# Kernel tuning notes

Hardware: AMD Instinct MI355X
Metric: run time of the kernel (lower is better)

## Reference

```python
import math
import jax, jax.numpy as jnp
import numpy as np

C_S, C_Z, N_HEAD, C, N_QP, N_PV = 384, 128, 12, 16, 4, 8
B, N_RES = 1, 512
OUT_IN = N_HEAD * (C + 3 * N_PV + N_PV + C_Z)  # 2112


def _quat_to_rot(q):
    # q: (..., 4) unit quaternions -> (..., 3, 3) rotation matrices
    w, x, y, z = q[..., 0], q[..., 1], q[..., 2], q[..., 3]
    R = jnp.stack([
        1 - 2 * (y * y + z * z), 2 * (x * y - w * z), 2 * (x * z + w * y),
        2 * (x * y + w * z), 1 - 2 * (x * x + z * z), 2 * (y * z - w * x),
        2 * (x * z - w * y), 2 * (y * z + w * x), 1 - 2 * (x * x + y * y),
    ], axis=-1)
    return R.reshape(q.shape[:-1] + (3, 3))


def setup_inputs() -> dict:
    key = jax.random.key(0)
    ks = jax.random.split(key, 16)
    s = jax.random.normal(ks[0], (B, N_RES, C_S), jnp.float32)
    z = jax.random.normal(ks[1], (B, N_RES, N_RES, C_Z), jnp.float32)
    # Valid rigid backbone transforms: random rotation + translation in 4x4 homogeneous form.
    quat = jax.random.normal(ks[2], (B, N_RES, 4), jnp.float32)
    quat = quat / jnp.linalg.norm(quat, axis=-1, keepdims=True)
    R = _quat_to_rot(quat)
    t = 10.0 * jax.random.normal(ks[3], (B, N_RES, 3), jnp.float32)
    T = jnp.zeros((B, N_RES, 4, 4), jnp.float32)
    T = T.at[..., :3, :3].set(R).at[..., :3, 3].set(t).at[..., 3, 3].set(1.0)
    sc = 0.02
    w_q = sc * jax.random.normal(ks[4], (C_S, N_HEAD * C), jnp.float32)
    w_k = sc * jax.random.normal(ks[5], (C_S, N_HEAD * C), jnp.float32)
    w_v = sc * jax.random.normal(ks[6], (C_S, N_HEAD * C), jnp.float32)
    w_qp = sc * jax.random.normal(ks[7], (C_S, N_HEAD * N_QP * 3), jnp.float32)
    w_kp = sc * jax.random.normal(ks[8], (C_S, N_HEAD * N_QP * 3), jnp.float32)
    w_vp = sc * jax.random.normal(ks[9], (C_S, N_HEAD * N_PV * 3), jnp.float32)
    w_b = sc * jax.random.normal(ks[10], (C_Z, N_HEAD), jnp.float32)
    gamma = 0.5 * jax.random.normal(ks[11], (N_HEAD,), jnp.float32)
    w_out = sc * jax.random.normal(ks[12], (OUT_IN, C_S), jnp.float32)
    b_out = jnp.zeros((C_S,), jnp.float32)
    return dict(s=s, z=z, T=T, w_q=w_q, w_k=w_k, w_v=w_v, w_qp=w_qp, w_kp=w_kp,
                w_vp=w_vp, w_b=w_b, gamma=gamma, w_out=w_out, b_out=b_out)


def _ipa(s, z, T, w_q, w_k, w_v, w_qp, w_kp, w_vp, w_b, gamma, w_out, b_out):
    b, n, _ = s.shape
    H, c, P, Pv = N_HEAD, C, N_QP, N_PV
    # qkv embeddings: (b, H, n, c)
    q = (s @ w_q).reshape(b, n, H, c).transpose(0, 2, 1, 3)
    k = (s @ w_k).reshape(b, n, H, c).transpose(0, 2, 1, 3)
    v = (s @ w_v).reshape(b, n, H, c).transpose(0, 2, 1, 3)
    # point embeddings: (b, H, P, n, 3)
    qp = (s @ w_qp).reshape(b, n, H, P, 3).transpose(0, 2, 3, 1, 4)
    kp = (s @ w_kp).reshape(b, n, H, P, 3).transpose(0, 2, 3, 1, 4)
    vp = (s @ w_vp).reshape(b, n, H, Pv, 3).transpose(0, 2, 3, 1, 4)
    R = T[..., :3, :3]                      # (b, n, 3, 3)
    t = T[..., :3, 3]                       # (b, n, 3)
    t_b = t[:, None, None, :, :]            # broadcast over (H, P)
    # global-frame points: T_i o x = R_i x + t_i
    qpg = jnp.einsum('bnxy,bhpny->bhpnx', R, qp) + t_b
    kpg = jnp.einsum('bnxy,bhpny->bhpnx', R, kp) + t_b
    vpg = jnp.einsum('bnxy,bhpny->bhpnx', R, vp) + t_b
    # attention logits (Alg 22 line 7)
    bias = jnp.einsum('bijz,zh->bhij', z, w_b)                      # pair bias
    dot = jnp.einsum('bhic,bhjc->bhij', q, k) * (1.0 / math.sqrt(c))
    diff = qpg[:, :, :, :, None, :] - kpg[:, :, :, None, :, :]       # (b,H,P,i,j,3)
    d2 = jnp.sum(diff * diff, axis=(2, 5))                           # (b,H,i,j)
    gamma_sp = jax.nn.softplus(gamma)[None, :, None, None]
    w_C = math.sqrt(2.0 / (9.0 * P))
    w_L = math.sqrt(1.0 / 3.0)
    a = jax.nn.softmax(w_L * (dot + bias - 0.5 * gamma_sp * w_C * d2), axis=-1)
    # outputs
    o = jnp.einsum('bhij,bhjc->bhic', a, v)                          # (b,H,n,c)
    opg = jnp.einsum('bhij,bhpjx->bhpix', a, vpg)                    # (b,H,Pv,n,3)
    # back to local frame: T_i^{-1} o x = R_i^T (x - t_i)
    op = jnp.einsum('bnxy,bhpnx->bhpny', R, opg - t_b)
    op_norm = jnp.sqrt(jnp.sum(op * op, axis=-1) + 1e-8)             # (b,H,Pv,n)
    o_pair = jnp.einsum('bhij,bijz->bhiz', a, z)                     # (b,H,n,c_z)
    o_f = o.transpose(0, 2, 1, 3).reshape(b, n, H * c)
    op_f = op.transpose(0, 3, 1, 2, 4).reshape(b, n, H * Pv * 3)
    norm_f = op_norm.transpose(0, 3, 1, 2).reshape(b, n, H * Pv)
    pair_f = o_pair.transpose(0, 2, 1, 3).reshape(b, n, H * C_Z)
    cat = jnp.concatenate([o_f, op_f, norm_f, pair_f], axis=-1)      # (b, n, OUT_IN)
    return cat @ w_out + b_out


def reference(s, z, T, w_q, w_k, w_v, w_qp, w_kp, w_vp, w_b, gamma, w_out, b_out):
    return _ipa(s, z, T, w_q, w_k, w_v, w_qp, w_kp, w_vp, w_b, gamma, w_out, b_out)
```

## Files before the change

kernel.cpp:

```cpp
#include <hip/hip_runtime.h>
#include <hip/hip_bf16.h>

typedef __attribute__((ext_vector_type(8))) short short8v;
typedef __attribute__((ext_vector_type(4))) float f32x4;

__device__ __forceinline__ short f2bf(float f){
  unsigned u = __builtin_bit_cast(unsigned, f);
  u += 0x7fffu + ((u >> 16) & 1u);
  return (short)(u >> 16);
}
__device__ __forceinline__ float bf2f(unsigned short s){
  unsigned u = ((unsigned)s) << 16;
  return __builtin_bit_cast(float, u);
}

__device__ __forceinline__ void gload16(const short* g, short* l){
  __builtin_amdgcn_global_load_lds(
    (const __attribute__((address_space(1))) unsigned int*)g,
    (__attribute__((address_space(3))) unsigned int*)l,
    16, 0, 0);
}

__global__ __launch_bounds__(256) void prep_kernel(
    const float* __restrict__ s, const float* __restrict__ w_b,
    const float* __restrict__ wq, const float* __restrict__ wk, const float* __restrict__ wv,
    const float* __restrict__ wqp, const float* __restrict__ wkp, const float* __restrict__ wvp,
    const float* __restrict__ w_out,
    short* __restrict__ s_bf, short* __restrict__ wbbf,
    short* __restrict__ WT, short* __restrict__ w_outT)
{
  __shared__ float tsh[64][65];
  int b = blockIdx.x;
  if (b < 192) {
    int gid = b*256 + threadIdx.x;
    float4 f = *(const float4*)(s + (size_t)gid*4);
    short4 o = make_short4(f2bf(f.x), f2bf(f.y), f2bf(f.z), f2bf(f.w));
    *(short4*)(s_bf + (size_t)gid*4) = o;
  } else if (b == 192) {
    const float wL = 0.57735026918962576f;
    for (int u = threadIdx.x; u < 2048; u += 256) {
      int h = u >> 7, zc = u & 127;
      float v = (h < 12) ? w_b[zc*12 + h]*wL : 0.f;
      wbbf[u] = f2bf(v);
    }
  } else if (b < 373) {
    int t = b - 193;
    int n0 = (t % 5)*64, k0 = ((t/5) % 6)*64, src = t/30;
    const float* in; int N; int rowoff;
    switch (src) {
      case 0: in = wq;  N = 192; rowoff = 0;   break;
      case 1: in = wk;  N = 192; rowoff = 192; break;
      case 2: in = wv;  N = 192; rowoff = 384; break;
      case 3: in = wqp; N = 144; rowoff = 576; break;
      case 4: in = wkp; N = 144; rowoff = 720; break;
      default:in = wvp; N = 288; rowoff = 864; break;
    }
    if (n0 >= N) return;
    int lx = threadIdx.x & 15, ly = threadIdx.x >> 4;
    #pragma unroll
    for (int p=0;p<4;++p){
      int r = ly + p*16, c = lx*4;
      float v0=0.f,v1=0.f,v2=0.f,v3=0.f;
      if (n0 + c + 3 < N) {
        float4 v = *(const float4*)(in + (size_t)(k0+r)*N + n0 + c);
        v0=v.x; v1=v.y; v2=v.z; v3=v.w;
      } else {
        if (n0+c+0 < N) v0 = in[(size_t)(k0+r)*N + n0+c+0];
        if (n0+c+1 < N) v1 = in[(size_t)(k0+r)*N + n0+c+1];
        if (n0+c+2 < N) v2 = in[(size_t)(k0+r)*N + n0+c+2];
        if (n0+c+3 < N) v3 = in[(size_t)(k0+r)*N + n0+c+3];
      }
      tsh[c+0][r]=v0; tsh[c+1][r]=v1; tsh[c+2][r]=v2; tsh[c+3][r]=v3;
    }
    __syncthreads();
    #pragma unroll
    for (int p=0;p<4;++p){
      int nr = ly + p*16, kc = lx*4;
      if (n0 + nr < N) {
        short4 o = make_short4(f2bf(tsh[nr][kc]), f2bf(tsh[nr][kc+1]),
                               f2bf(tsh[nr][kc+2]), f2bf(tsh[nr][kc+3]));
        *(short4*)(WT + (size_t)(rowoff+n0+nr)*384 + k0 + kc) = o;
      }
    }
  } else {
    int t = b - 373;
    int n0 = (t % 6)*64, k0 = (t/6)*64;
    int lx = threadIdx.x & 15, ly = threadIdx.x >> 4;
    #pragma unroll
    for (int p=0;p<4;++p){
      int r = ly + p*16, c = lx*4;
      float4 v = *(const float4*)(w_out + (size_t)(k0+r)*384 + n0 + c);
      tsh[c+0][r]=v.x; tsh[c+1][r]=v.y; tsh[c+2][r]=v.z; tsh[c+3][r]=v.w;
    }
    __syncthreads();
    #pragma unroll
    for (int p=0;p<4;++p){
      int nr = ly + p*16, kc = lx*4;
      short4 o = make_short4(f2bf(tsh[nr][kc]), f2bf(tsh[nr][kc+1]),
                             f2bf(tsh[nr][kc+2]), f2bf(tsh[nr][kc+3]));
      *(short4*)(w_outT + (size_t)(n0+nr)*2112 + k0 + kc) = o;
    }
  }
}

__global__ __launch_bounds__(256) void gemm_bf16_kernel(
    const short* __restrict__ A, const short* __restrict__ BT,
    float* __restrict__ C, const float* __restrict__ bias,
    int M, int N, int K)
{
  __shared__ __align__(16) short As[2][4096];
  __shared__ __align__(16) short Bs[2][4096];
  int tid = threadIdx.x;
  int n0 = blockIdx.x*128, m0 = blockIdx.y*128;
  int w = tid >> 6, lane = tid & 63;
  int wr = w >> 1, wc = w & 1;
  int lrow = lane & 15, kg = lane >> 4;
  int nt = K >> 5;
  f32x4 acc[4][4] = {};

  const short* Abase = A  + (size_t)m0*K;
  const short* Bbase = BT + (size_t)n0*K;
  int sr = tid >> 2, scc = (tid & 3)*8;

  auto stage = [&](int b, int k0){
    const short* Ab = Abase + k0;
    const short* Bb = Bbase + k0;
    gload16(Ab + (size_t)sr*K + scc,      &As[b][tid*8]);
    gload16(Bb + (size_t)sr*K + scc,      &Bs[b][tid*8]);
    gload16(Ab + (size_t)(sr+64)*K + scc, &As[b][2048 + tid*8]);
    gload16(Bb + (size_t)(sr+64)*K + scc, &Bs[b][2048 + tid*8]);
  };

  stage(0, 0);
  for (int kt = 0; kt < nt; ++kt){
    int cb = kt & 1;
    if (kt + 1 < nt){
      stage(cb ^ 1, (kt+1) << 5);
      asm volatile("s_waitcnt vmcnt(4)" ::: "memory");
    } else {
      asm volatile("s_waitcnt vmcnt(0)" ::: "memory");
    }
    __builtin_amdgcn_s_barrier();
    short8v af[4], bfr[4];
    #pragma unroll
    for (int mi=0; mi<4; ++mi)
      af[mi]  = *(const short8v*)&As[cb][(wr*64 + mi*16 + lrow)*32 + kg*8];
    #pragma unroll
    for (int ni=0; ni<4; ++ni)
      bfr[ni] = *(const short8v*)&Bs[cb][(wc*64 + ni*16 + lrow)*32 + kg*8];
    #pragma unroll
    for (int mi=0; mi<4; ++mi)
      #pragma unroll
      for (int ni=0; ni<4; ++ni)
        acc[mi][ni] = __builtin_amdgcn_mfma_f32_16x16x32_bf16(af[mi], bfr[ni], acc[mi][ni], 0, 0, 0);
    __builtin_amdgcn_s_barrier();
  }

  #pragma unroll
  for (int mi=0; mi<4; ++mi)
    #pragma unroll
    for (int ni=0; ni<4; ++ni) {
      int col = n0 + wc*64 + ni*16 + lrow;
      float bv = bias ? bias[col] : 0.f;
      #pragma unroll
      for (int jj=0; jj<4; ++jj) {
        int row = m0 + wr*64 + mi*16 + kg*4 + jj;
        C[(size_t)row*N + col] = acc[mi][ni][jj] + bv;
      }
    }
}

__global__ __launch_bounds__(256) void gemm_splitk_kernel(
    const short* __restrict__ A, const short* __restrict__ BT,
    float* __restrict__ Cpart, int M, int N, int lda, int Kc)
{
  __shared__ __align__(16) short As[2][4096];
  __shared__ __align__(16) short Bs[2][4096];
  int tid = threadIdx.x;
  int n0 = blockIdx.x*128, m0 = blockIdx.y*128;
  int kb = blockIdx.z;
  int w = tid >> 6, lane = tid & 63;
  int wr = w >> 1, wc = w & 1;
  int lrow = lane & 15, kg = lane >> 4;
  int nt = Kc >> 5;
  f32x4 acc[4][4] = {};

  const short* Abase = A  + (size_t)m0*lda + (size_t)kb*Kc;
  const short* Bbase = BT + (size_t)n0*lda + (size_t)kb*Kc;
  int sr = tid >> 2, scc = (tid & 3)*8;

  auto stage = [&](int b, int k0){
    const short* Ab = Abase + k0;
    const short* Bb = Bbase + k0;
    gload16(Ab + (size_t)sr*lda + scc,      &As[b][tid*8]);
    gload16(Bb + (size_t)sr*lda + scc,      &Bs[b][tid*8]);
    gload16(Ab + (size_t)(sr+64)*lda + scc, &As[b][2048 + tid*8]);
    gload16(Bb + (size_t)(sr+64)*lda + scc, &Bs[b][2048 + tid*8]);
  };

  stage(0, 0);
  for (int kt = 0; kt < nt; ++kt){
    int cb = kt & 1;
    if (kt + 1 < nt){
      stage(cb ^ 1, (kt+1) << 5);
      asm volatile("s_waitcnt vmcnt(4)" ::: "memory");
    } else {
      asm volatile("s_waitcnt vmcnt(0)" ::: "memory");
    }
    __builtin_amdgcn_s_barrier();
    short8v af[4], bfr[4];
    #pragma unroll
    for (int mi=0; mi<4; ++mi)
      af[mi]  = *(const short8v*)&As[cb][(wr*64 + mi*16 + lrow)*32 + kg*8];
    #pragma unroll
    for (int ni=0; ni<4; ++ni)
      bfr[ni] = *(const short8v*)&Bs[cb][(wc*64 + ni*16 + lrow)*32 + kg*8];
    #pragma unroll
    for (int mi=0; mi<4; ++mi)
      #pragma unroll
      for (int ni=0; ni<4; ++ni)
        acc[mi][ni] = __builtin_amdgcn_mfma_f32_16x16x32_bf16(af[mi], bfr[ni], acc[mi][ni], 0, 0, 0);
    __builtin_amdgcn_s_barrier();
  }

  float* Cp = Cpart + (size_t)kb*M*N;
  #pragma unroll
  for (int mi=0; mi<4; ++mi)
    #pragma unroll
    for (int ni=0; ni<4; ++ni) {
      int col = n0 + wc*64 + ni*16 + lrow;
      #pragma unroll
      for (int jj=0; jj<4; ++jj) {
        int row = m0 + wr*64 + mi*16 + kg*4 + jj;
        Cp[(size_t)row*N + col] = acc[mi][ni][jj];
      }
    }
}

__global__ __launch_bounds__(256) void reduce6_kernel(
    const float* __restrict__ Cpart, const float* __restrict__ bias,
    float* __restrict__ out)
{
  int idx = blockIdx.x*256 + threadIdx.x;
  float v = bias[idx % 384];
  #pragma unroll
  for (int zc = 0; zc < 6; ++zc) v += Cpart[(size_t)zc*196608 + idx];
  out[idx] = v;
}

__global__ __launch_bounds__(256) void transform_kernel(
    const float* __restrict__ P, const float* __restrict__ T,
    float* __restrict__ kT, float* __restrict__ kpgT,
    float* __restrict__ qpg, unsigned short* __restrict__ vcatT)
{
  __shared__ float Ps[8][1160];
  __shared__ float Ts[8][12];
  int tid = threadIdx.x;
  int j0 = blockIdx.x*8;
  for (int u = tid; u < 8*288; u += 256) {
    int r = u / 288, c4 = u % 288;
    *(float4*)&Ps[r][c4*4] = *(const float4*)(P + (size_t)(j0+r)*1152 + c4*4);
  }
  if (tid < 96) {
    int r = tid / 12, e = tid % 12;
    Ts[r][e] = (e < 9) ? T[(j0+r)*16 + (e/3)*4 + (e%3)]
                       : T[(j0+r)*16 + (e-9)*4 + 3];
  }
  __syncthreads();
  for (int u = tid; u < 1536; u += 256) {
    int row = u >> 3, jl = u & 7;
    kT[(size_t)row*512 + j0 + jl] = Ps[jl][192 + row];
  }
  for (int u = tid; u < 1152; u += 256) {
    int e = u >> 3, jl = u & 7;
    int x = e % 3, hp = e / 3;
    const float* R = &Ts[jl][0];
    float kx = Ps[jl][720+hp*3], ky = Ps[jl][720+hp*3+1], kz = Ps[jl][720+hp*3+2];
    kpgT[(size_t)e*512 + j0 + jl] = R[x*3]*kx + R[x*3+1]*ky + R[x*3+2]*kz + Ts[jl][9+x];
  }
  for (int u = tid; u < 1152; u += 256) {
    int jl = u / 144, e = u % 144;
    int x = e % 3, hp = e / 3;
    const float* R = &Ts[jl][0];
    float qx = Ps[jl][576+hp*3], qy = Ps[jl][576+hp*3+1], qz = Ps[jl][576+hp*3+2];
    qpg[(size_t)(j0+jl)*144 + e] = R[x*3]*qx + R[x*3+1]*qy + R[x*3+2]*qz + Ts[jl][9+x];
  }
  for (int u = tid; u < 3840; u += 256) {
    int d = u >> 3, jl = u & 7;
    float val;
    if (d < 192) val = Ps[jl][384 + d];
    else {
      int e = d - 192;
      int x = e % 3, hp = e / 3;
      const float* R = &Ts[jl][0];
      float vx = Ps[jl][864+hp*3], vy = Ps[jl][864+hp*3+1], vz = Ps[jl][864+hp*3+2];
      val = R[x*3]*vx + R[x*3+1]*vy + R[x*3+2]*vz + Ts[jl][9+x];
    }
    vcatT[(size_t)d*512 + j0 + jl] = (unsigned short)f2bf(val);
  }
}

__global__ __launch_bounds__(256) void attn_part_kernel(
    const float* __restrict__ P, const float* __restrict__ qpg,
    const float* __restrict__ kT, const float* __restrict__ kpgT,
    const short* __restrict__ wbbf, const float* __restrict__ z,
    const unsigned short* __restrict__ vcatT,
    const float* __restrict__ gamma, float* __restrict__ part)
{
  __shared__ short zbT[16384];
  __shared__ float sc[12][132];
  __shared__ float qrow[192], qpgrow[144], gsp[12];
  int bid = blockIdx.x;
  int i = bid >> 2, jq = bid & 3;
  int j0 = jq * 128;
  int tid = threadIdx.x;
  float* pb = part + (size_t)bid * 2048;
  const float* zslab = z + (size_t)i*65536 + (size_t)j0*128;

  if (tid < 192) qrow[tid] = P[(size_t)i*1152 + tid];
  if (tid < 144) qpgrow[tid] = qpg[(size_t)i*144 + tid];
  if (tid < 12)  { float g = gamma[tid]; gsp[tid] = log1pf(__expf(g)); }

  {
    int q = tid & 31, jb = tid >> 5;
    for (int r = 0; r < 16; ++r) {
      int jj = jb + r*8;
      float4 f = *(const float4*)(zslab + (size_t)jj*128 + q*4);
      short wv0 = f2bf(f.x), wv1 = f2bf(f.y), wv2 = f2bf(f.z), wv3 = f2bf(f.w);
      int jc = jj >> 3, jr = jj & 7;
      int zc = q*4;
      zbT[(zc+0)*128 + ((jc ^ (((zc+0)&15)^((zc+0)>>4))) << 3) + jr] = wv0;
      zbT[(zc+1)*128 + ((jc ^ (((zc+1)&15)^((zc+1)>>4))) << 3) + jr] = wv1;
      zbT[(zc+2)*128 + ((jc ^ (((zc+2)&15)^((zc+2)>>4))) << 3) + jr] = wv2;
      zbT[(zc+3)*128 + ((jc ^ (((zc+3)&15)^((zc+3)>>4))) << 3) + jr] = wv3;
    }
  }

  {
    int w = tid >> 6, lane = tid & 63;
    int lrow = lane & 15, kg = lane >> 4;
    #pragma unroll
    for (int sub = 0; sub < 2; ++sub) {
      int m = w*2 + sub;
      const float* zr = zslab + (size_t)(m*16 + lrow)*128;
      f32x4 acc = {0.f,0.f,0.f,0.f};
      #pragma unroll
      for (int ks = 0; ks < 4; ++ks) {
        int c0 = ks*32 + kg*8;
        float4 z0 = *(const float4*)(zr + c0);
        float4 z1 = *(const float4*)(zr + c0 + 4);
        short8v af;
        af[0]=f2bf(z0.x); af[1]=f2bf(z0.y); af[2]=f2bf(z0.z); af[3]=f2bf(z0.w);
        af[4]=f2bf(z1.x); af[5]=f2bf(z1.y); af[6]=f2bf(z1.z); af[7]=f2bf(z1.w);
        short8v bfv = *(const short8v*)(wbbf + lrow*128 + c0);
        acc = __builtin_amdgcn_mfma_f32_16x16x32_bf16(af, bfv, acc, 0, 0, 0);
      }
      if (lrow < 12) {
        #pragma unroll
        for (int r=0;r<4;++r)
          sc[lrow][m*16 + kg*4 + r] = acc[r];
      }
    }
  }
  __syncthreads();

  {
    int j = tid & 127, hh = tid >> 7;
    const float wL = 0.57735026918962576f;
    const float wC = 0.23570226039551584f;
    #pragma unroll
    for (int hl = 0; hl < 6; ++hl) {
      int h = hh*6 + hl;
      float dot = 0.f;
      #pragma unroll
      for (int c=0;c<16;++c) dot += qrow[h*16+c] * kT[(size_t)(h*16+c)*512 + j0 + j];
      float d2 = 0.f;
      #pragma unroll
      for (int e=0;e<12;++e){ float d = qpgrow[h*12+e] - kpgT[(size_t)(h*12+e)*512 + j0 + j]; d2 += d*d; }
      sc[h][j] += wL*(dot*0.25f - 0.5f*gsp[h]*wC*d2);
    }
  }
  __syncthreads();

  if (tid < 192) {
    int h = tid >> 4, l = tid & 15;
    float v[8]; float m = -1e30f;
    #pragma unroll
    for (int u=0;u<8;++u){ v[u] = sc[h][l + u*16]; m = fmaxf(m, v[u]); }
    #pragma unroll
    for (int s2=1;s2<16;s2<<=1) m = fmaxf(m, __shfl_xor(m, s2));
    float sum = 0.f;
    #pragma unroll
    for (int u=0;u<8;++u){ v[u] = __expf(v[u]-m); sum += v[u]; sc[h][l + u*16] = v[u]; }
    #pragma unroll
    for (int s2=1;s2<16;s2<<=1) sum += __shfl_xor(sum, s2);
    if (l == 0) { pb[h] = m; pb[12+h] = sum; }
  }
  __syncthreads();

  if (tid < 240) {
    #pragma unroll
    for (int rr=0; rr<2; ++rr) {
      int d = tid + rr*240;
      int h = (d < 192) ? (d >> 4) : ((d - 192) / 24);
      const unsigned short* vp = vcatT + (size_t)d*512 + j0;
      float s = 0.f;
      #pragma unroll 4
      for (int jc = 0; jc < 16; ++jc) {
        short8v vv = *(const short8v*)(vp + jc*8);
        float4 a0 = *(const float4*)&sc[h][jc*8];
        float4 a1 = *(const float4*)&sc[h][jc*8+4];
        s += a0.x*bf2f((unsigned short)vv[0]) + a0.y*bf2f((unsigned short)vv[1])
           + a0.z*bf2f((unsigned short)vv[2]) + a0.w*bf2f((unsigned short)vv[3])
           + a1.x*bf2f((unsigned short)vv[4]) + a1.y*bf2f((unsigned short)vv[5])
           + a1.z*bf2f((unsigned short)vv[6]) + a1.w*bf2f((unsigned short)vv[7]);
      }
      pb[24 + d] = s;
    }
  }

  {
    int w = tid >> 6, lane = tid & 63;
    int lrow = lane & 15, kg = lane >> 4;
    short8v afr[4];
    #pragma unroll
    for (int ks = 0; ks < 4; ++ks) {
      int row = lrow < 12 ? lrow : 11;
      const float* sp = &sc[row][ks*32 + kg*8];
      float4 a0 = *(const float4*)sp;
      float4 a1 = *(const float4*)(sp+4);
      short8v a;
      a[0]=f2bf(a0.x); a[1]=f2bf(a0.y); a[2]=f2bf(a0.z); a[3]=f2bf(a0.w);
      a[4]=f2bf(a1.x); a[5]=f2bf(a1.y); a[6]=f2bf(a1.z); a[7]=f2bf(a1.w);
      afr[ks] = a;
    }
    #pragma unroll
    for (int t = 0; t < 2; ++t) {
      int zc = w*32 + t*16 + lrow;
      int sw = (zc & 15) ^ (zc >> 4);
      f32x4 pacc = {0.f,0.f,0.f,0.f};
      #pragma unroll
      for (int ks = 0; ks < 4; ++ks) {
        int chunk = (ks*4 + kg) ^ sw;
        short8v bfv = *(const short8v*)&zbT[zc*128 + (chunk<<3)];
        pacc = __builtin_amdgcn_mfma_f32_16x16x32_bf16(afr[ks], bfv, pacc, 0, 0, 0);
      }
      if (kg < 3) {
        #pragma unroll
        for (int r = 0; r < 4; ++r) {
          int h = kg*4 + r;
          pb[512 + h*128 + zc] = pacc[r];
        }
      }
    }
  }
}

__global__ __launch_bounds__(256) void combine_kernel(
    const float* __restrict__ part, const float* __restrict__ T,
    short* __restrict__ cat)
{
  __shared__ float w4[4][12], inv[12];
  __shared__ float opgf[288];
  __shared__ float Ri[9], ti[3];
  int i = blockIdx.x, tid = threadIdx.x;
  const float* pb = part + (size_t)i * 4 * 2048;

  if (tid < 12) {
    float m0 = pb[tid], m1 = pb[2048+tid], m2 = pb[4096+tid], m3 = pb[6144+tid];
    float mh = fmaxf(fmaxf(m0,m1), fmaxf(m2,m3));
    float w0 = __expf(m0-mh), w1 = __expf(m1-mh), w2 = __expf(m2-mh), w3 = __expf(m3-mh);
    float S = w0*pb[12+tid] + w1*pb[2060+tid] + w2*pb[4108+tid] + w3*pb[6156+tid];
    w4[0][tid]=w0; w4[1][tid]=w1; w4[2][tid]=w2; w4[3][tid]=w3;
    inv[tid] = 1.f/S;
  }
  if (tid >= 64 && tid < 73) { int e = tid-64; Ri[e] = T[i*16 + (e/3)*4 + (e%3)]; }
  if (tid >= 76 && tid < 79) { int e = tid-76; ti[e] = T[i*16 + e*4 + 3]; }
  __syncthreads();

  short* crow = cat + (size_t)i*2112;

  if (tid < 192) {
    int h = tid >> 4;
    float v = w4[0][h]*pb[24+tid] + w4[1][h]*pb[2072+tid]
            + w4[2][h]*pb[4120+tid] + w4[3][h]*pb[6168+tid];
    crow[tid] = f2bf(v * inv[h]);
  }
  for (int u = tid; u < 288; u += 256) {
    int h = u / 24;
    float v = w4[0][h]*pb[216+u] + w4[1][h]*pb[2264+u]
            + w4[2][h]*pb[4312+u] + w4[3][h]*pb[6360+u];
    opgf[u] = v * inv[h];
  }
  __syncthreads();
  if (tid < 96) {
    float d0 = opgf[tid*3+0]-ti[0], d1 = opgf[tid*3+1]-ti[1], d2v = opgf[tid*3+2]-ti[2];
    float o0 = Ri[0]*d0 + Ri[3]*d1 + Ri[6]*d2v;
    float o1 = Ri[1]*d0 + Ri[4]*d1 + Ri[7]*d2v;
    float o2 = Ri[2]*d0 + Ri[5]*d1 + Ri[8]*d2v;
    crow[192+tid*3+0] = f2bf(o0); crow[192+tid*3+1] = f2bf(o1); crow[192+tid*3+2] = f2bf(o2);
    crow[480+tid] = f2bf(sqrtf(o0*o0 + o1*o1 + o2*o2 + 1e-8f));
  }
  for (int u = tid; u < 1536; u += 256) {
    int h = u >> 7;
    float v = w4[0][h]*pb[512+u] + w4[1][h]*pb[2560+u]
            + w4[2][h]*pb[4608+u] + w4[3][h]*pb[6656+u];
    crow[576+u] = f2bf(v * inv[h]);
  }
}

extern "C" void kernel_launch(void* const* d_in, const int* in_sizes, int n_in,
                              void* d_out, int out_size, void* d_ws, size_t ws_size,
                              hipStream_t stream) {
  const float* s     = (const float*)d_in[0];
  const float* z     = (const float*)d_in[1];
  const float* T     = (const float*)d_in[2];
  const float* w_q   = (const float*)d_in[3];
  const float* w_k   = (const float*)d_in[4];
  const float* w_v   = (const float*)d_in[5];
  const float* w_qp  = (const float*)d_in[6];
  const float* w_kp  = (const float*)d_in[7];
  const float* w_vp  = (const float*)d_in[8];
  const float* w_b   = (const float*)d_in[9];
  const float* gamma = (const float*)d_in[10];
  const float* w_out = (const float*)d_in[11];
  const float* b_out = (const float*)d_in[12];

  float* ws = (float*)d_ws;
  float* P      = ws;
  float* kT     = ws + 589824;
  float* kpgT   = ws + 688128;
  float* qpg    = ws + 761856;
  short* wbbf   = (short*)(ws + 835584);
  short* s_bf   = (short*)(ws + 836608);
  short* WT     = (short*)(ws + 934912);
  short* w_outT = (short*)(ws + 1156096);
  unsigned short* vcatT = (unsigned short*)(ws + 1561600);
  short* cat    = (short*)(ws + 1684480);
  float* partb  = ws + 2225152;
  float* Cpart  = ws + 6419456;

  prep_kernel<<<571, 256, 0, stream>>>(s, w_b, w_q, w_k, w_v, w_qp, w_kp, w_vp, w_out,
                                       s_bf, wbbf, WT, w_outT);
  gemm_bf16_kernel<<<dim3(9,4), 256, 0, stream>>>(s_bf, WT, P, nullptr, 512, 1152, 384);
  transform_kernel<<<64, 256, 0, stream>>>(P, T, kT, kpgT, qpg, vcatT);
  attn_part_kernel<<<2048, 256, 0, stream>>>(P, qpg, kT, kpgT, wbbf, z, vcatT, gamma, partb);
  combine_kernel<<<512, 256, 0, stream>>>(partb, T, cat);
  gemm_splitk_kernel<<<dim3(3,4,6), 256, 0, stream>>>(cat, w_outT, Cpart, 512, 384, 2112, 352);
  reduce6_kernel<<<768, 256, 0, stream>>>(Cpart, b_out, (float*)d_out);
}
```

Baseline: 116.9 us.

## Replace LDS-transposed bf16 MFMA pair path with direct fp32 z reduction

Drops the bf16 transposed z tile in LDS and its MFMA pair-output contraction. Instead, each thread reads fp32 z columns straight from global memory and accumulates all 12 heads in registers, then two half-slabs are summed through shared memory. The v-concat buffer is relaid out j-major (padded to 512), so the attention-value sum reads coalesced across lanes. This frees a large LDS buffer and removes the conversion and swizzle work, but moves the pair contraction from MFMA to scalar FMAs and rereads z from global memory.

```diff
diff --git a/kernel.cpp b/kernel.cpp
--- a/kernel.cpp
+++ b/kernel.cpp
@@ -251,7 +251,7 @@
 __global__ __launch_bounds__(256) void transform_kernel(
     const float* __restrict__ P, const float* __restrict__ T,
     float* __restrict__ kT, float* __restrict__ kpgT,
-    float* __restrict__ qpg, unsigned short* __restrict__ vcatT)
+    float* __restrict__ qpg, unsigned short* __restrict__ vcatJ)
 {
   __shared__ float Ps[8][1160];
   __shared__ float Ts[8][12];
@@ -285,18 +285,18 @@
     float qx = Ps[jl][576+hp*3], qy = Ps[jl][576+hp*3+1], qz = Ps[jl][576+hp*3+2];
     qpg[(size_t)(j0+jl)*144 + e] = R[x*3]*qx + R[x*3+1]*qy + R[x*3+2]*qz + Ts[jl][9+x];
   }
-  for (int u = tid; u < 3840; u += 256) {
-    int d = u >> 3, jl = u & 7;
-    float val;
+  for (int u = tid; u < 4096; u += 256) {
+    int jl = u >> 9, d = u & 511;
+    float val = 0.f;
     if (d < 192) val = Ps[jl][384 + d];
-    else {
+    else if (d < 480) {
       int e = d - 192;
       int x = e % 3, hp = e / 3;
       const float* R = &Ts[jl][0];
       float vx = Ps[jl][864+hp*3], vy = Ps[jl][864+hp*3+1], vz = Ps[jl][864+hp*3+2];
       val = R[x*3]*vx + R[x*3+1]*vy + R[x*3+2]*vz + Ts[jl][9+x];
     }
-    vcatT[(size_t)d*512 + j0 + jl] = (unsigned short)f2bf(val);
+    vcatJ[(size_t)(j0+jl)*512 + d] = (unsigned short)f2bf(val);
   }
 }
 
@@ -304,16 +304,18 @@
     const float* __restrict__ P, const float* __restrict__ qpg,
     const float* __restrict__ kT, const float* __restrict__ kpgT,
     const short* __restrict__ wbbf, const float* __restrict__ z,
-    const unsigned short* __restrict__ vcatT,
+    const unsigned short* __restrict__ vcatJ,
     const float* __restrict__ gamma, float* __restrict__ part)
 {
-  __shared__ short zbT[16384];
   __shared__ float sc[12][132];
+  __shared__ float pairpart[2][12][128];
   __shared__ float qrow[192], qpgrow[144], gsp[12];
   int bid = blockIdx.x;
   int i = bid >> 2, jq = bid & 3;
   int j0 = jq * 128;
   int tid = threadIdx.x;
+  int w = tid >> 6, lane = tid & 63;
+  int lrow = lane & 15, kg = lane >> 4;
   float* pb = part + (size_t)bid * 2048;
   const float* zslab = z + (size_t)i*65536 + (size_t)j0*128;
 
@@ -322,23 +324,6 @@
   if (tid < 12)  { float g = gamma[tid]; gsp[tid] = log1pf(__expf(g)); }
 
   {
-    int q = tid & 31, jb = tid >> 5;
-    for (int r = 0; r < 16; ++r) {
-      int jj = jb + r*8;
-      float4 f = *(const float4*)(zslab + (size_t)jj*128 + q*4);
-      short wv0 = f2bf(f.x), wv1 = f2bf(f.y), wv2 = f2bf(f.z), wv3 = f2bf(f.w);
-      int jc = jj >> 3, jr = jj & 7;
-      int zc = q*4;
-      zbT[(zc+0)*128 + ((jc ^ (((zc+0)&15)^((zc+0)>>4))) << 3) + jr] = wv0;
-      zbT[(zc+1)*128 + ((jc ^ (((zc+1)&15)^((zc+1)>>4))) << 3) + jr] = wv1;
-      zbT[(zc+2)*128 + ((jc ^ (((zc+2)&15)^((zc+2)>>4))) << 3) + jr] = wv2;
-      zbT[(zc+3)*128 + ((jc ^ (((zc+3)&15)^((zc+3)>>4))) << 3) + jr] = wv3;
-    }
-  }
-
-  {
-    int w = tid >> 6, lane = tid & 63;
-    int lrow = lane & 15, kg = lane >> 4;
     #pragma unroll
     for (int sub = 0; sub < 2; ++sub) {
       int m = w*2 + sub;
@@ -398,61 +383,47 @@
   }
   __syncthreads();
 
-  if (tid < 240) {
-    #pragma unroll
-    for (int rr=0; rr<2; ++rr) {
-      int d = tid + rr*240;
-      int h = (d < 192) ? (d >> 4) : ((d - 192) / 24);
-      const unsigned short* vp = vcatT + (size_t)d*512 + j0;
-      float s = 0.f;
+  {
+    int zc = tid & 127, jh = tid >> 7;
+    const float* zb = zslab + (size_t)jh*64*128 + zc;
+    float acc[12] = {};
+    for (int g = 0; g < 16; ++g) {
+      int jj = jh*64 + g*4;
+      float zv0 = zb[(size_t)(g*4+0)*128];
+      float zv1 = zb[(size_t)(g*4+1)*128];
+      float zv2 = zb[(size_t)(g*4+2)*128];
+      float zv3 = zb[(size_t)(g*4+3)*128];
+      #pragma unroll
+      for (int h=0; h<12; ++h) {
+        float4 a = *(const float4*)&sc[h][jj];
+        acc[h] += a.x*zv0 + a.y*zv1 + a.z*zv2 + a.w*zv3;
+      }
+    }
+    #pragma unroll
+    for (int h=0; h<12; ++h) pairpart[jh][h][zc] = acc[h];
+  }
+
+  {
+    #pragma unroll
+    for (int cc = 0; cc < 2; ++cc) {
+      int ch = w + cc*4;
+      int d = ch*64 + lane;
+      int h = (d < 192) ? (d >> 4) : ((d < 480) ? (d - 192) / 24 : 11);
+      const unsigned short* vj = vcatJ + (size_t)j0*512 + d;
+      float a0 = 0.f, a1 = 0.f;
       #pragma unroll 4
-      for (int jc = 0; jc < 16; ++jc) {
-        short8v vv = *(const short8v*)(vp + jc*8);
-        float4 a0 = *(const float4*)&sc[h][jc*8];
-        float4 a1 = *(const float4*)&sc[h][jc*8+4];
-        s += a0.x*bf2f((unsigned short)vv[0]) + a0.y*bf2f((unsigned short)vv[1])
-           + a0.z*bf2f((unsigned short)vv[2]) + a0.w*bf2f((unsigned short)vv[3])
-           + a1.x*bf2f((unsigned short)vv[4]) + a1.y*bf2f((unsigned short)vv[5])
-           + a1.z*bf2f((unsigned short)vv[6]) + a1.w*bf2f((unsigned short)vv[7]);
-      }
-      pb[24 + d] = s;
-    }
-  }
-
-  {
-    int w = tid >> 6, lane = tid & 63;
-    int lrow = lane & 15, kg = lane >> 4;
-    short8v afr[4];
-    #pragma unroll
-    for (int ks = 0; ks < 4; ++ks) {
-      int row = lrow < 12 ? lrow : 11;
-      const float* sp = &sc[row][ks*32 + kg*8];
-      float4 a0 = *(const float4*)sp;
-      float4 a1 = *(const float4*)(sp+4);
-      short8v a;
-      a[0]=f2bf(a0.x); a[1]=f2bf(a0.y); a[2]=f2bf(a0.z); a[3]=f2bf(a0.w);
-      a[4]=f2bf(a1.x); a[5]=f2bf(a1.y); a[6]=f2bf(a1.z); a[7]=f2bf(a1.w);
-      afr[ks] = a;
-    }
-    #pragma unroll
-    for (int t = 0; t < 2; ++t) {
-      int zc = w*32 + t*16 + lrow;
-      int sw = (zc & 15) ^ (zc >> 4);
-      f32x4 pacc = {0.f,0.f,0.f,0.f};
-      #pragma unroll
-      for (int ks = 0; ks < 4; ++ks) {
-        int chunk = (ks*4 + kg) ^ sw;
-        short8v bfv = *(const short8v*)&zbT[zc*128 + (chunk<<3)];
-        pacc = __builtin_amdgcn_mfma_f32_16x16x32_bf16(afr[ks], bfv, pacc, 0, 0, 0);
-      }
-      if (kg < 3) {
-        #pragma unroll
-        for (int r = 0; r < 4; ++r) {
-          int h = kg*4 + r;
-          pb[512 + h*128 + zc] = pacc[r];
-        }
-      }
-    }
+      for (int j = 0; j < 128; j += 2) {
+        a0 += sc[h][j]   * bf2f(vj[(size_t)j*512]);
+        a1 += sc[h][j+1] * bf2f(vj[(size_t)(j+1)*512]);
+      }
+      if (d < 480) pb[24 + d] = a0 + a1;
+    }
+  }
+  __syncthreads();
+
+  for (int u = tid; u < 1536; u += 256) {
+    int h = u >> 7, zc = u & 127;
+    pb[512 + u] = pairpart[0][h][zc] + pairpart[1][h][zc];
   }
 }
 
@@ -535,16 +506,16 @@
   short* s_bf   = (short*)(ws + 836608);
   short* WT     = (short*)(ws + 934912);
   short* w_outT = (short*)(ws + 1156096);
-  unsigned short* vcatT = (unsigned short*)(ws + 1561600);
-  short* cat    = (short*)(ws + 1684480);
-  float* partb  = ws + 2225152;
-  float* Cpart  = ws + 6419456;
+  unsigned short* vcatJ = (unsigned short*)(ws + 1561600);
+  short* cat    = (short*)(ws + 1692672);
+  float* partb  = ws + 2233344;
+  float* Cpart  = ws + 6427648;
 
   prep_kernel<<<571, 256, 0, stream>>>(s, w_b, w_q, w_k, w_v, w_qp, w_kp, w_vp, w_out,
                                        s_bf, wbbf, WT, w_outT);
   gemm_bf16_kernel<<<dim3(9,4), 256, 0, stream>>>(s_bf, WT, P, nullptr, 512, 1152, 384);
-  transform_kernel<<<64, 256, 0, stream>>>(P, T, kT, kpgT, qpg, vcatT);
-  attn_part_kernel<<<2048, 256, 0, stream>>>(P, qpg, kT, kpgT, wbbf, z, vcatT, gamma, partb);
+  transform_kernel<<<64, 256, 0, stream>>>(P, T, kT, kpgT, qpg, vcatJ);
+  attn_part_kernel<<<2048, 256, 0, stream>>>(P, qpg, kT, kpgT, wbbf, z, vcatJ, gamma, partb);
   combine_kernel<<<512, 256, 0, stream>>>(partb, T, cat);
   gemm_splitk_kernel<<<dim3(3,4,6), 256, 0, stream>>>(cat, w_outT, Cpart, 512, 384, 2112, 352);
   reduce6_kernel<<<768, 256, 0, stream>>>(Cpart, b_out, (float*)d_out);
```

Result: slower. 126.9 us (+8.6%).

## Store V concatenation row-major per key and split a·V across all four waves

Applied to the files above, without the earlier changes.

The V/VP concatenation is now written key-major with each head's 40 values contiguous and padded to 512 columns, replacing the feature-major transposed layout. In the attention kernel all four waves each take 32 keys, with every lane accumulating 8 contiguous features, instead of 240 threads each walking a strided feature row. Per-wave partial sums are reduced through a new 8 KB shared buffer after an extra barrier, and the combine kernel indexes the new padded layout. The aim is coalesced global loads and use of all threads, at the cost of more LDS use (which may lower occupancy) and an added synchronization.

```diff
diff --git a/kernel.cpp b/kernel.cpp
--- a/kernel.cpp
+++ b/kernel.cpp
@@ -251,7 +251,7 @@
 __global__ __launch_bounds__(256) void transform_kernel(
     const float* __restrict__ P, const float* __restrict__ T,
     float* __restrict__ kT, float* __restrict__ kpgT,
-    float* __restrict__ qpg, unsigned short* __restrict__ vcatT)
+    float* __restrict__ qpg, unsigned short* __restrict__ vcatH)
 {
   __shared__ float Ps[8][1160];
   __shared__ float Ts[8][12];
@@ -285,18 +285,22 @@
     float qx = Ps[jl][576+hp*3], qy = Ps[jl][576+hp*3+1], qz = Ps[jl][576+hp*3+2];
     qpg[(size_t)(j0+jl)*144 + e] = R[x*3]*qx + R[x*3+1]*qy + R[x*3+2]*qz + Ts[jl][9+x];
   }
-  for (int u = tid; u < 3840; u += 256) {
-    int d = u >> 3, jl = u & 7;
-    float val;
-    if (d < 192) val = Ps[jl][384 + d];
-    else {
-      int e = d - 192;
-      int x = e % 3, hp = e / 3;
-      const float* R = &Ts[jl][0];
-      float vx = Ps[jl][864+hp*3], vy = Ps[jl][864+hp*3+1], vz = Ps[jl][864+hp*3+2];
-      val = R[x*3]*vx + R[x*3+1]*vy + R[x*3+2]*vz + Ts[jl][9+x];
-    }
-    vcatT[(size_t)d*512 + j0 + jl] = (unsigned short)f2bf(val);
+  for (int u = tid; u < 4096; u += 256) {
+    int jl = u >> 9, dn = u & 511;
+    float val = 0.f;
+    if (dn < 480) {
+      int h = dn / 40, c = dn % 40;
+      if (c < 16) {
+        val = Ps[jl][384 + h*16 + c];
+      } else {
+        int e = c - 16;
+        int x = e % 3, hp = e / 3;
+        const float* R = &Ts[jl][0];
+        float vx = Ps[jl][864+h*24+hp*3], vy = Ps[jl][864+h*24+hp*3+1], vz = Ps[jl][864+h*24+hp*3+2];
+        val = R[x*3]*vx + R[x*3+1]*vy + R[x*3+2]*vz + Ts[jl][9+x];
+      }
+    }
+    vcatH[(size_t)(j0+jl)*512 + dn] = (unsigned short)f2bf(val);
   }
 }
 
@@ -304,11 +308,12 @@
     const float* __restrict__ P, const float* __restrict__ qpg,
     const float* __restrict__ kT, const float* __restrict__ kpgT,
     const short* __restrict__ wbbf, const float* __restrict__ z,
-    const unsigned short* __restrict__ vcatT,
+    const unsigned short* __restrict__ vcatH,
     const float* __restrict__ gamma, float* __restrict__ part)
 {
   __shared__ short zbT[16384];
   __shared__ float sc[12][132];
+  __shared__ float ppart[4][512];
   __shared__ float qrow[192], qpgrow[144], gsp[12];
   int bid = blockIdx.x;
   int i = bid >> 2, jq = bid & 3;
@@ -398,25 +403,20 @@
   }
   __syncthreads();
 
-  if (tid < 240) {
-    #pragma unroll
-    for (int rr=0; rr<2; ++rr) {
-      int d = tid + rr*240;
-      int h = (d < 192) ? (d >> 4) : ((d - 192) / 24);
-      const unsigned short* vp = vcatT + (size_t)d*512 + j0;
-      float s = 0.f;
-      #pragma unroll 4
-      for (int jc = 0; jc < 16; ++jc) {
-        short8v vv = *(const short8v*)(vp + jc*8);
-        float4 a0 = *(const float4*)&sc[h][jc*8];
-        float4 a1 = *(const float4*)&sc[h][jc*8+4];
-        s += a0.x*bf2f((unsigned short)vv[0]) + a0.y*bf2f((unsigned short)vv[1])
-           + a0.z*bf2f((unsigned short)vv[2]) + a0.w*bf2f((unsigned short)vv[3])
-           + a1.x*bf2f((unsigned short)vv[4]) + a1.y*bf2f((unsigned short)vv[5])
-           + a1.z*bf2f((unsigned short)vv[6]) + a1.w*bf2f((unsigned short)vv[7]);
-      }
-      pb[24 + d] = s;
-    }
+  {
+    int w = tid >> 6, lane = tid & 63;
+    int hc = (lane < 60) ? (lane / 5) : 11;
+    float acc[8] = {};
+    const unsigned short* base = vcatH + (size_t)(j0 + w*32)*512 + lane*8;
+    #pragma unroll 4
+    for (int jj = 0; jj < 32; ++jj) {
+      short8v vv = *(const short8v*)(base + (size_t)jj*512);
+      float a = sc[hc][w*32 + jj];
+      #pragma unroll
+      for (int e=0;e<8;++e) acc[e] += a * bf2f((unsigned short)vv[e]);
+    }
+    #pragma unroll
+    for (int e=0;e<8;++e) ppart[w][lane*8+e] = acc[e];
   }
 
   {
@@ -454,6 +454,15 @@
       }
     }
   }
+  __syncthreads();
+
+  if (tid < 240) {
+    #pragma unroll
+    for (int rr=0; rr<2; ++rr) {
+      int d = tid + rr*240;
+      pb[24 + d] = ppart[0][d] + ppart[1][d] + ppart[2][d] + ppart[3][d];
+    }
+  }
 }
 
 __global__ __launch_bounds__(256) void combine_kernel(
@@ -481,15 +490,17 @@
   short* crow = cat + (size_t)i*2112;
 
   if (tid < 192) {
-    int h = tid >> 4;
-    float v = w4[0][h]*pb[24+tid] + w4[1][h]*pb[2072+tid]
-            + w4[2][h]*pb[4120+tid] + w4[3][h]*pb[6168+tid];
+    int h = tid >> 4, c = tid & 15;
+    int dn = 40*h + c;
+    float v = w4[0][h]*pb[24+dn] + w4[1][h]*pb[2072+dn]
+            + w4[2][h]*pb[4120+dn] + w4[3][h]*pb[6168+dn];
     crow[tid] = f2bf(v * inv[h]);
   }
   for (int u = tid; u < 288; u += 256) {
-    int h = u / 24;
-    float v = w4[0][h]*pb[216+u] + w4[1][h]*pb[2264+u]
-            + w4[2][h]*pb[4312+u] + w4[3][h]*pb[6360+u];
+    int h = u / 24, e = u % 24;
+    int dn = 40*h + 16 + e;
+    float v = w4[0][h]*pb[24+dn] + w4[1][h]*pb[2072+dn]
+            + w4[2][h]*pb[4120+dn] + w4[3][h]*pb[6168+dn];
     opgf[u] = v * inv[h];
   }
   __syncthreads();
@@ -535,16 +546,16 @@
   short* s_bf   = (short*)(ws + 836608);
   short* WT     = (short*)(ws + 934912);
   short* w_outT = (short*)(ws + 1156096);
-  unsigned short* vcatT = (unsigned short*)(ws + 1561600);
-  short* cat    = (short*)(ws + 1684480);
-  float* partb  = ws + 2225152;
-  float* Cpart  = ws + 6419456;
+  unsigned short* vcatH = (unsigned short*)(ws + 1561600);
+  short* cat    = (short*)(ws + 1692672);
+  float* partb  = ws + 2233344;
+  float* Cpart  = ws + 6427648;
 
   prep_kernel<<<571, 256, 0, stream>>>(s, w_b, w_q, w_k, w_v, w_qp, w_kp, w_vp, w_out,
                                        s_bf, wbbf, WT, w_outT);
   gemm_bf16_kernel<<<dim3(9,4), 256, 0, stream>>>(s_bf, WT, P, nullptr, 512, 1152, 384);
-  transform_kernel<<<64, 256, 0, stream>>>(P, T, kT, kpgT, qpg, vcatT);
-  attn_part_kernel<<<2048, 256, 0, stream>>>(P, qpg, kT, kpgT, wbbf, z, vcatT, gamma, partb);
+  transform_kernel<<<64, 256, 0, stream>>>(P, T, kT, kpgT, qpg, vcatH);
+  attn_part_kernel<<<2048, 256, 0, stream>>>(P, qpg, kT, kpgT, wbbf, z, vcatH, gamma, partb);
   combine_kernel<<<512, 256, 0, stream>>>(partb, T, cat);
   gemm_splitk_kernel<<<dim3(3,4,6), 256, 0, stream>>>(cat, w_outT, Cpart, 512, 384, 2112, 352);
   reduce6_kernel<<<768, 256, 0, stream>>>(Cpart, b_out, (float*)d_out);
```

After: 105.6 us. -9.6%, faster.
